# Kernel optimization log

Measured on AMD Instinct MI355X. Metric: run time of the kernel, lower is better.

The kernel has to match this reference:

```python
import jax, jax.numpy as jnp
import numpy as np

N = 100000      # nodes
E = 1600000     # edges (avg degree 16)
DIN = 128
DH = 128
DOUT = 64
K = 2           # SGConv propagation steps
EPS = 1e-5      # BatchNorm eps


def setup_inputs() -> dict:
    key = jax.random.key(0)
    ks = jax.random.split(key, 12)
    x = jax.random.normal(ks[0], (N, DIN), dtype=jnp.float32)
    edge_index = jax.random.randint(ks[1], (2, E), 0, N, dtype=jnp.int32)
    def lin(k, fin, fout):
        k1, k2 = jax.random.split(k)
        s = 1.0 / np.sqrt(fin)
        W = jax.random.uniform(k1, (fin, fout), jnp.float32, -s, s)
        b = jax.random.uniform(k2, (fout,), jnp.float32, -s, s)
        return W, b
    W1, b1 = lin(ks[2], DIN, DH)
    W2, b2 = lin(ks[3], DH, DH)
    W3, b3 = lin(ks[4], DH, DOUT)
    g1 = jnp.ones((DH,), jnp.float32); be1 = jnp.zeros((DH,), jnp.float32)
    g2 = jnp.ones((DH,), jnp.float32); be2 = jnp.zeros((DH,), jnp.float32)
    return {"x": x, "edge_index": edge_index,
            "W1": W1, "b1": b1, "g1": g1, "be1": be1,
            "W2": W2, "b2": b2, "g2": g2, "be2": be2,
            "W3": W3, "b3": b3}


def _sgc_propagate(h, row, col, norm):
    # h: [N, d]; gather source nodes, scale per-edge, scatter-add to dest
    for _ in range(K):
        msg = norm[:, None] * h[row]                      # [E, d]
        h = jax.ops.segment_sum(msg, col, num_segments=N)  # [N, d]
    return h


def _batchnorm(h, gamma, beta):
    # training-mode BN over node axis, biased variance (torch semantics)
    mu = jnp.mean(h, axis=0)
    var = jnp.mean(jnp.square(h - mu), axis=0)
    return gamma * (h - mu) * jax.lax.rsqrt(var + EPS) + beta


def reference(x, edge_index, W1, b1, g1, be1, W2, b2, g2, be2, W3, b3):
    row, col = edge_index[0], edge_index[1]
    # symmetric degree normalization; degree counted on row (as in source)
    deg = jax.ops.segment_sum(jnp.ones((E,), x.dtype), row, num_segments=N)
    dis = jnp.where(deg > 0, 1.0 / jnp.sqrt(jnp.maximum(deg, 1.0)), 0.0)
    norm = dis[row] * dis[col]                             # [E]

    h = _sgc_propagate(x, row, col, norm)
    h = _batchnorm(h @ W1 + b1, g1, be1)   # dropout p=0.0 -> identity
    h = _sgc_propagate(h, row, col, norm)
    h = _batchnorm(h @ W2 + b2, g2, be2)
    return h @ W3 + b3                      # [N, DOUT]
```

## Files before the change

### kernel.cpp

```cpp
#include <hip/hip_runtime.h>


typedef __attribute__((ext_vector_type(8))) short bf16x8;
typedef __attribute__((ext_vector_type(4))) float f32x4;

#define RBITS 12
#define RSIZE (1 << RBITS)
#define NRANGE 25
#define NCHUNK 100
#define RSTRIDE (NRANGE * RSIZE)
#define SLOTS 64

static inline size_t align256(size_t x) { return (x + 255) & ~(size_t)255; }

__device__ inline unsigned short bf16rn(float f) {
    unsigned int u = __builtin_bit_cast(unsigned int, f);
    u += 0x7fffu + ((u >> 16) & 1u);
    return (unsigned short)(u >> 16);
}
__device__ inline float bflo(unsigned int u) { return __builtin_bit_cast(float, u << 16); }
__device__ inline float bfhi(unsigned int u) { return __builtin_bit_cast(float, u & 0xffff0000u); }
__device__ inline unsigned int packbf2(float a, float b) {
    return (unsigned int)bf16rn(a) | ((unsigned int)bf16rn(b) << 16);
}

__global__ void hist_row_kernel(const int* __restrict__ row, int E,
                                int* __restrict__ staging) {
    __shared__ int lcnt[RSIZE];
    int range = blockIdx.x % NRANGE;
    int chunk = blockIdx.x / NRANGE;
    for (int i = threadIdx.x; i < RSIZE; i += 256) lcnt[i] = 0;
    __syncthreads();
    int lo = range << RBITS;
    int ebeg = (int)((long long)E * chunk / NCHUNK);
    int eend = (int)((long long)E * (chunk + 1) / NCHUNK);
    for (int i = ebeg + threadIdx.x * 4; i + 3 < eend; i += 256 * 4) {
        int4 v = *(const int4*)(row + i);
        unsigned a;
        a = (unsigned)(v.x - lo); if (a < RSIZE) atomicAdd(&lcnt[a], 1);
        a = (unsigned)(v.y - lo); if (a < RSIZE) atomicAdd(&lcnt[a], 1);
        a = (unsigned)(v.z - lo); if (a < RSIZE) atomicAdd(&lcnt[a], 1);
        a = (unsigned)(v.w - lo); if (a < RSIZE) atomicAdd(&lcnt[a], 1);
    }
    __syncthreads();
    int* dst = staging + chunk * RSTRIDE + lo;
    for (int i = threadIdx.x; i < RSIZE; i += 256) dst[i] = lcnt[i];
}

__global__ void dis_kernel(const int* __restrict__ staging, float* __restrict__ dis, int n) {
    int i = blockIdx.x * blockDim.x + threadIdx.x;
    if (i < n) {
        int d = 0;
#pragma unroll 4
        for (int c = 0; c < NCHUNK; ++c) d += staging[c * RSTRIDE + i];
        dis[i] = d > 0 ? rsqrtf((float)d) : 0.f;
    }
}

__global__ void bucket_fill_kernel(const int* __restrict__ row, const int* __restrict__ col,
                                   const float* __restrict__ dis,
                                   int* __restrict__ fcnt, int2* __restrict__ bucket, int E) {
    int e = blockIdx.x * blockDim.x + threadIdx.x;
    if (e < E) {
        int r = row[e], c = col[e];
        int slot = atomicAdd(&fcnt[c], 1);
        if (slot < SLOTS) {
            int2 v;
            v.x = r;
            v.y = __float_as_int(dis[r] * dis[c]);
            bucket[(size_t)c * SLOTS + slot] = v;
        }
    }
}


__global__ void xcvt_kernel(const float* __restrict__ x, unsigned int* __restrict__ x16, int total4) {
    for (int i = blockIdx.x * blockDim.x + threadIdx.x; i < total4; i += gridDim.x * blockDim.x) {
        float4 f = ((const float4*)x)[i];
        x16[i * 2] = packbf2(f.x, f.y);
        x16[i * 2 + 1] = packbf2(f.z, f.w);
    }
}

__global__ void wcvt_kernel(const float* __restrict__ W1, const float* __restrict__ W2,
                            unsigned short* __restrict__ W1t, unsigned short* __restrict__ W2t) {
    int i = blockIdx.x * blockDim.x + threadIdx.x;
    if (i < 32768) {
        const float* W = (i < 16384) ? W1 : W2;
        unsigned short* T = (i < 16384) ? W1t : W2t;
        int j = i & 16383;
        int k = j >> 7, c = j & 127;
        T[c * 128 + k] = bf16rn(W[j]);
    }
}


template <bool AFF>
__global__ void spmm16_kernel(const int* __restrict__ fcnt, const int2* __restrict__ bucket,
                              const unsigned short* __restrict__ h_in,
                              const float* __restrict__ scale, const float* __restrict__ shift,
                              unsigned short* __restrict__ h_out, int n) {
    int gw = __builtin_amdgcn_readfirstlane((blockIdx.x * blockDim.x + threadIdx.x) >> 6);
    int lane = threadIdx.x & 63;
    int sub = lane & 15;
    int grp = lane >> 4;
    if (gw >= n) return;
    uint4* outp = (uint4*)(h_out + (size_t)gw * 128) + sub;
    int cnt = fcnt[gw];
    cnt = cnt < SLOTS ? cnt : SLOTS;
    if (cnt == 0) {
        if (lane < 16) {
            uint4 z = {0u, 0u, 0u, 0u};
            *outp = z;
        }
        return;
    }
    const int2* base = bucket + (size_t)gw * SLOTS;
    float acc[8];
#pragma unroll
    for (int j = 0; j < 8; ++j) acc[j] = 0.f;
    float sc[8], sh[8];
    if (AFF) {
        float4 s0 = ((const float4*)scale)[sub * 2];
        float4 s1 = ((const float4*)scale)[sub * 2 + 1];
        float4 h0 = ((const float4*)shift)[sub * 2];
        float4 h1 = ((const float4*)shift)[sub * 2 + 1];
        sc[0] = s0.x; sc[1] = s0.y; sc[2] = s0.z; sc[3] = s0.w;
        sc[4] = s1.x; sc[5] = s1.y; sc[6] = s1.z; sc[7] = s1.w;
        sh[0] = h0.x; sh[1] = h0.y; sh[2] = h0.z; sh[3] = h0.w;
        sh[4] = h1.x; sh[5] = h1.y; sh[6] = h1.z; sh[7] = h1.w;
    }
    bool g1 = (grp & 1) != 0;
    bool g2 = (grp & 2) != 0;
    for (int j0 = 0; j0 < cnt; j0 += 16) {
        int2 ent[16];
#pragma unroll
        for (int k = 0; k < 16; ++k) ent[k] = base[j0 + k];
        uint4 u[4];
        float wsel[4];
#pragma unroll
        for (int k = 0; k < 4; ++k) {
            int i0 = j0 + 4 * k;
            int e0 = (i0 + 0 < cnt) ? ent[4 * k + 0].x : 0;
            int e1 = (i0 + 1 < cnt) ? ent[4 * k + 1].x : 0;
            int e2 = (i0 + 2 < cnt) ? ent[4 * k + 2].x : 0;
            int e3 = (i0 + 3 < cnt) ? ent[4 * k + 3].x : 0;
            float w0 = (i0 + 0 < cnt) ? __int_as_float(ent[4 * k + 0].y) : 0.f;
            float w1 = (i0 + 1 < cnt) ? __int_as_float(ent[4 * k + 1].y) : 0.f;
            float w2 = (i0 + 2 < cnt) ? __int_as_float(ent[4 * k + 2].y) : 0.f;
            float w3 = (i0 + 3 < cnt) ? __int_as_float(ent[4 * k + 3].y) : 0.f;
            int eA = g1 ? e1 : e0;
            int eB = g1 ? e3 : e2;
            int esel = g2 ? eB : eA;
            float wA = g1 ? w1 : w0;
            float wB = g1 ? w3 : w2;
            wsel[k] = g2 ? wB : wA;
            u[k] = *(const uint4*)(h_in + (size_t)esel * 128 + sub * 8);
        }
#pragma unroll
        for (int k = 0; k < 4; ++k) {
            float w = wsel[k];
            unsigned int uu[4] = {u[k].x, u[k].y, u[k].z, u[k].w};
#pragma unroll
            for (int q = 0; q < 4; ++q) {
                float f0 = bflo(uu[q]), f1 = bfhi(uu[q]);
                if (AFF) {
                    f0 = fmaf(sc[2 * q], f0, sh[2 * q]);
                    f1 = fmaf(sc[2 * q + 1], f1, sh[2 * q + 1]);
                }
                acc[2 * q] = fmaf(w, f0, acc[2 * q]);
                acc[2 * q + 1] = fmaf(w, f1, acc[2 * q + 1]);
            }
        }
    }
#pragma unroll
    for (int j = 0; j < 8; ++j) {
        acc[j] += __shfl_xor(acc[j], 16, 64);
        acc[j] += __shfl_xor(acc[j], 32, 64);
    }
    if (lane < 16) {
        uint4 o;
        o.x = packbf2(acc[0], acc[1]);
        o.y = packbf2(acc[2], acc[3]);
        o.z = packbf2(acc[4], acc[5]);
        o.w = packbf2(acc[6], acc[7]);
        *outp = o;
    }
}


template <int NCT, bool OUTF32, bool STATS>
__launch_bounds__(256)
__global__ void gemm16_kernel(const unsigned short* __restrict__ X,
                              const unsigned short* __restrict__ Wt,
                              const float* __restrict__ bias, void* __restrict__ Y,
                              float* __restrict__ gsum, float* __restrict__ gsq, int n) {
    __shared__ __align__(16) char lds[NCT * 16 * 256];
    __shared__ float ssum[NCT * 16], ssq[NCT * 16];
    for (int i = threadIdx.x; i < NCT * 16 * 16; i += 256) {
        int col = i >> 4;
        int kbyte = (i & 15) << 4;
        *(uint4*)(lds + col * 256 + (kbyte ^ ((col & 7) << 4))) = ((const uint4*)Wt)[i];
    }
    if (STATS) {
        for (int i = threadIdx.x; i < NCT * 16; i += 256) {
            ssum[i] = 0.f;
            ssq[i] = 0.f;
        }
    }
    __syncthreads();

    int lane = threadIdx.x & 63;
    int wave = threadIdx.x >> 6;
    int cl = lane & 15, g = lane >> 4;

    bf16x8 b[NCT][4];
#pragma unroll
    for (int ct = 0; ct < NCT; ++ct) {
        int col = ct * 16 + cl;
#pragma unroll
        for (int kc = 0; kc < 4; ++kc) {
            int kbyte = kc * 64 + g * 16;
            b[ct][kc] = *(const bf16x8*)(lds + col * 256 + (kbyte ^ ((col & 7) << 4)));
        }
    }
    float bc[NCT];
#pragma unroll
    for (int ct = 0; ct < NCT; ++ct) bc[ct] = bias[ct * 16 + cl];

    for (int rb0 = blockIdx.x * 64; rb0 < n; rb0 += gridDim.x * 64) {
        int rb = rb0 + wave * 16;
        if (rb >= n) continue;
        int row = rb + cl;
        int rowc = row < n ? row : n - 1;
        const unsigned short* xr = X + (size_t)rowc * 128;
        bf16x8 a[4];
#pragma unroll
        for (int kc = 0; kc < 4; ++kc) a[kc] = *(const bf16x8*)(xr + kc * 32 + g * 8);
#pragma unroll
        for (int ct = 0; ct < NCT; ++ct) {
            f32x4 acc = {bc[ct], bc[ct], bc[ct], bc[ct]};
#pragma unroll
            for (int kc = 0; kc < 4; ++kc)
                acc = __builtin_amdgcn_mfma_f32_16x16x32_bf16(a[kc], b[ct][kc], acc, 0, 0, 0);
            int colo = ct * 16 + cl;
            if (STATS) {
                float s = acc[0] + acc[1] + acc[2] + acc[3];
                float q = acc[0] * acc[0] + acc[1] * acc[1] + acc[2] * acc[2] + acc[3] * acc[3];
                s += __shfl_xor(s, 16, 64);
                s += __shfl_xor(s, 32, 64);
                q += __shfl_xor(q, 16, 64);
                q += __shfl_xor(q, 32, 64);
                if (g == 0) {
                    atomicAdd(&ssum[colo], s);
                    atomicAdd(&ssq[colo], q);
                }
            }
#pragma unroll
            for (int i = 0; i < 4; ++i) {
                int ro = rb + g * 4 + i;
                if (ro < n) {
                    if (OUTF32)
                        ((float*)Y)[(size_t)ro * (NCT * 16) + colo] = acc[i];
                    else
                        ((unsigned short*)Y)[(size_t)ro * 128 + colo] = bf16rn(acc[i]);
                }
            }
        }
    }
    if (STATS) {
        __syncthreads();
        for (int i = threadIdx.x; i < NCT * 16; i += 256) {
            atomicAdd(&gsum[i], ssum[i]);
            atomicAdd(&gsq[i], ssq[i]);
        }
    }
}


__global__ void bn_final_kernel(const float* __restrict__ gsum, const float* __restrict__ gsq,
                                const float* __restrict__ gamma, const float* __restrict__ beta,
                                int n, float* __restrict__ scale, float* __restrict__ shift) {
    int c = threadIdx.x;
    if (c < 128) {
        float fn = (float)n;
        float mu = gsum[c] / fn;
        float var = gsq[c] / fn - mu * mu;
        float inv = rsqrtf(var + 1e-5f);
        float sc = gamma[c] * inv;
        scale[c] = sc;
        shift[c] = beta[c] - sc * mu;
    }
}

__global__ void fold_w3_kernel(const float* __restrict__ W3, const float* __restrict__ b3,
                               const float* __restrict__ scale, const float* __restrict__ shift,
                               unsigned short* __restrict__ W3t, float* __restrict__ b3f) {
    int c = threadIdx.x;
    if (c < 64) {
        float acc = b3[c];
        for (int k = 0; k < 128; ++k) {
            float w = W3[k * 64 + c];
            W3t[c * 128 + k] = bf16rn(scale[k] * w);
            acc += shift[k] * w;
        }
        b3f[c] = acc;
    }
}


extern "C" void kernel_launch(void* const* d_in, const int* in_sizes, int n_in,
                              void* d_out, int out_size, void* d_ws, size_t ws_size,
                              hipStream_t stream) {
    const float* x = (const float*)d_in[0];
    const int* edge = (const int*)d_in[1];
    const float* W1 = (const float*)d_in[2];
    const float* b1 = (const float*)d_in[3];
    const float* g1 = (const float*)d_in[4];
    const float* be1 = (const float*)d_in[5];
    const float* W2 = (const float*)d_in[6];
    const float* b2 = (const float*)d_in[7];
    const float* g2 = (const float*)d_in[8];
    const float* be2 = (const float*)d_in[9];
    const float* W3 = (const float*)d_in[10];
    const float* b3 = (const float*)d_in[11];
    float* out = (float*)d_out;

    const int N = in_sizes[0] / 128;
    const int E = in_sizes[1] / 2;
    const int* erow = edge;
    const int* ecol = edge + E;

    char* p = (char*)d_ws;
    size_t off = 0;
    auto carve = [&](size_t bytes) {
        void* r = p + off;
        off += align256(bytes);
        return r;
    };
    unsigned short* x16 = (unsigned short*)carve((size_t)N * 128 * 2);
    unsigned short* A16 = (unsigned short*)carve((size_t)N * 128 * 2);
    unsigned short* B16 = (unsigned short*)carve((size_t)N * 128 * 2);
    int2* bucket = (int2*)carve((size_t)N * SLOTS * 8);
    int* fcnt = (int*)carve((size_t)N * 4);
    float* dis = (float*)carve((size_t)N * 4);
    float* gsum = (float*)carve(1024);
    float* gsq = (float*)(gsum + 128);
    float* scale1 = (float*)carve(512);
    float* shift1 = (float*)carve(512);
    float* scale2 = (float*)carve(512);
    float* shift2 = (float*)carve(512);
    unsigned short* W1t = (unsigned short*)carve(128 * 128 * 2);
    unsigned short* W2t = (unsigned short*)carve(128 * 128 * 2);
    unsigned short* W3t = (unsigned short*)carve(64 * 128 * 2);
    float* b3f = (float*)carve(256);
    int* staging = (int*)bucket;
    (void)ws_size;

    const int TB = 256;
    const int gE = (E + TB - 1) / TB;
    const int gN = (N + TB - 1) / TB;
    const int gSp = (N + 3) / 4;
    const int gGemm = (N + 63) / 64;
    const int gGemmS = 320;

    hipMemsetAsync(fcnt, 0, (size_t)N * 4, stream);
    hist_row_kernel<<<NRANGE * NCHUNK, TB, 0, stream>>>(erow, E, staging);
    dis_kernel<<<gN, TB, 0, stream>>>(staging, dis, N);
    bucket_fill_kernel<<<gE, TB, 0, stream>>>(erow, ecol, dis, fcnt, bucket, E);

    xcvt_kernel<<<2048, TB, 0, stream>>>(x, (unsigned int*)x16, N * 32);
    wcvt_kernel<<<128, TB, 0, stream>>>(W1, W2, W1t, W2t);

    spmm16_kernel<false><<<gSp, TB, 0, stream>>>(fcnt, bucket, x16, nullptr, nullptr, A16, N);
    spmm16_kernel<false><<<gSp, TB, 0, stream>>>(fcnt, bucket, A16, nullptr, nullptr, B16, N);

    hipMemsetAsync(gsum, 0, 1024, stream);
    gemm16_kernel<8, false, true><<<gGemmS, TB, 0, stream>>>(B16, W1t, b1, A16, gsum, gsq, N);
    bn_final_kernel<<<1, 128, 0, stream>>>(gsum, gsq, g1, be1, N, scale1, shift1);

    spmm16_kernel<true><<<gSp, TB, 0, stream>>>(fcnt, bucket, A16, scale1, shift1, B16, N);
    spmm16_kernel<false><<<gSp, TB, 0, stream>>>(fcnt, bucket, B16, nullptr, nullptr, A16, N);

    hipMemsetAsync(gsum, 0, 1024, stream);
    gemm16_kernel<8, false, true><<<gGemmS, TB, 0, stream>>>(A16, W2t, b2, B16, gsum, gsq, N);
    bn_final_kernel<<<1, 128, 0, stream>>>(gsum, gsq, g2, be2, N, scale2, shift2);

    fold_w3_kernel<<<1, 64, 0, stream>>>(W3, b3, scale2, shift2, W3t, b3f);
    gemm16_kernel<4, true, false><<<gGemm, TB, 0, stream>>>(B16, W3t, b3f, out, nullptr, nullptr, N);
}
```

Measured before the change: 463.7 us.

## Build compact CSR via two-pass partition sort instead of fixed-slot buckets

Replaces the atomic fixed-slot (64 per node) bucket fill with a two-level counting sort: a per-chunk histogram over coarse column buckets, a scan, a scatter into partitions, then a per-bucket local sort that writes a dense CSR with per-edge norms. The SpMM kernels then read contiguous CSR ranges instead of padded slot arrays, which removes global atomics on per-node counters, the memset, and the sparse padded reads. It also drops the 64-edge cap, so high-degree nodes are no longer silently truncated. The row-degree histogram now packs two 16-bit counts per shared word, so each block covers a larger node range and fewer blocks are launched. In exchange it adds several extra kernel launches, including a single-block scan that runs serially.

```diff
diff --git a/kernel.cpp b/kernel.cpp
--- a/kernel.cpp
+++ b/kernel.cpp
@@ -4,12 +4,14 @@
 typedef __attribute__((ext_vector_type(8))) short bf16x8;
 typedef __attribute__((ext_vector_type(4))) float f32x4;
 
-#define RBITS 12
-#define RSIZE (1 << RBITS)
-#define NRANGE 25
-#define NCHUNK 100
-#define RSTRIDE (NRANGE * RSIZE)
-#define SLOTS 64
+#define HR_RBITS 14
+#define HR_RSIZE 16384
+#define HR_NRANGE 7
+#define HR_NCHUNK 100
+#define HR_WPC (HR_NRANGE * HR_RSIZE / 2)
+
+#define PA_NCHUNK 256
+#define PB_SHIFT 8
 
 static inline size_t align256(size_t x) { return (x + 255) & ~(size_t)255; }
 
@@ -25,51 +27,131 @@
 }
 
 __global__ void hist_row_kernel(const int* __restrict__ row, int E,
-                                int* __restrict__ staging) {
-    __shared__ int lcnt[RSIZE];
-    int range = blockIdx.x % NRANGE;
-    int chunk = blockIdx.x / NRANGE;
-    for (int i = threadIdx.x; i < RSIZE; i += 256) lcnt[i] = 0;
-    __syncthreads();
-    int lo = range << RBITS;
-    int ebeg = (int)((long long)E * chunk / NCHUNK);
-    int eend = (int)((long long)E * (chunk + 1) / NCHUNK);
+                                unsigned int* __restrict__ staging) {
+    __shared__ unsigned int l32[HR_RSIZE / 2];
+    int range = blockIdx.x % HR_NRANGE;
+    int chunk = blockIdx.x / HR_NRANGE;
+    for (int i = threadIdx.x; i < HR_RSIZE / 2; i += 256) l32[i] = 0;
+    __syncthreads();
+    int lo = range << HR_RBITS;
+    int ebeg = (int)((long long)E * chunk / HR_NCHUNK);
+    int eend = (int)((long long)E * (chunk + 1) / HR_NCHUNK);
     for (int i = ebeg + threadIdx.x * 4; i + 3 < eend; i += 256 * 4) {
         int4 v = *(const int4*)(row + i);
         unsigned a;
-        a = (unsigned)(v.x - lo); if (a < RSIZE) atomicAdd(&lcnt[a], 1);
-        a = (unsigned)(v.y - lo); if (a < RSIZE) atomicAdd(&lcnt[a], 1);
-        a = (unsigned)(v.z - lo); if (a < RSIZE) atomicAdd(&lcnt[a], 1);
-        a = (unsigned)(v.w - lo); if (a < RSIZE) atomicAdd(&lcnt[a], 1);
-    }
-    __syncthreads();
-    int* dst = staging + chunk * RSTRIDE + lo;
-    for (int i = threadIdx.x; i < RSIZE; i += 256) dst[i] = lcnt[i];
-}
-
-__global__ void dis_kernel(const int* __restrict__ staging, float* __restrict__ dis, int n) {
+        a = (unsigned)(v.x - lo); if (a < HR_RSIZE) atomicAdd(&l32[a >> 1], (a & 1) ? 0x10000u : 1u);
+        a = (unsigned)(v.y - lo); if (a < HR_RSIZE) atomicAdd(&l32[a >> 1], (a & 1) ? 0x10000u : 1u);
+        a = (unsigned)(v.z - lo); if (a < HR_RSIZE) atomicAdd(&l32[a >> 1], (a & 1) ? 0x10000u : 1u);
+        a = (unsigned)(v.w - lo); if (a < HR_RSIZE) atomicAdd(&l32[a >> 1], (a & 1) ? 0x10000u : 1u);
+    }
+    __syncthreads();
+    unsigned int* dst = staging + (size_t)chunk * HR_WPC + (lo >> 1);
+    for (int i = threadIdx.x; i < HR_RSIZE / 2; i += 256) dst[i] = l32[i];
+}
+
+__global__ void dis_kernel(const unsigned int* __restrict__ staging, float* __restrict__ dis, int n) {
     int i = blockIdx.x * blockDim.x + threadIdx.x;
     if (i < n) {
+        int shift = (i & 1) * 16;
         int d = 0;
 #pragma unroll 4
-        for (int c = 0; c < NCHUNK; ++c) d += staging[c * RSTRIDE + i];
+        for (int c = 0; c < HR_NCHUNK; ++c)
+            d += (staging[(size_t)c * HR_WPC + (i >> 1)] >> shift) & 0xffff;
         dis[i] = d > 0 ? rsqrtf((float)d) : 0.f;
     }
 }
 
-__global__ void bucket_fill_kernel(const int* __restrict__ row, const int* __restrict__ col,
-                                   const float* __restrict__ dis,
-                                   int* __restrict__ fcnt, int2* __restrict__ bucket, int E) {
-    int e = blockIdx.x * blockDim.x + threadIdx.x;
-    if (e < E) {
-        int r = row[e], c = col[e];
-        int slot = atomicAdd(&fcnt[c], 1);
-        if (slot < SLOTS) {
-            int2 v;
-            v.x = r;
-            v.y = __float_as_int(dis[r] * dis[c]);
-            bucket[(size_t)c * SLOTS + slot] = v;
-        }
+
+__global__ void pa_hist_kernel(const int* __restrict__ col, int E,
+                               int* __restrict__ chunkhist, int nbuck) {
+    __shared__ int lh[512];
+    int chunk = blockIdx.x;
+    for (int i = threadIdx.x; i < nbuck; i += 256) lh[i] = 0;
+    __syncthreads();
+    int ebeg = (int)((long long)E * chunk / PA_NCHUNK);
+    int eend = (int)((long long)E * (chunk + 1) / PA_NCHUNK);
+    for (int i = ebeg + threadIdx.x; i < eend; i += 256)
+        atomicAdd(&lh[col[i] >> PB_SHIFT], 1);
+    __syncthreads();
+    for (int i = threadIdx.x; i < nbuck; i += 256)
+        chunkhist[i * PA_NCHUNK + chunk] = lh[i];
+}
+
+__global__ void pa_scan_kernel(int* __restrict__ chunkhist, int* __restrict__ bucketstart,
+                               int nbuck) {
+    __shared__ int tot[512];
+    int b = threadIdx.x;
+    if (b < nbuck) {
+        int run = 0;
+        int* p = chunkhist + b * PA_NCHUNK;
+        for (int c = 0; c < PA_NCHUNK; ++c) { int v = p[c]; p[c] = run; run += v; }
+        tot[b] = run;
+    }
+    __syncthreads();
+    if (threadIdx.x == 0) {
+        int run = 0;
+        for (int i = 0; i < nbuck; ++i) { bucketstart[i] = run; run += tot[i]; }
+        bucketstart[nbuck] = run;
+    }
+    __syncthreads();
+    if (b < nbuck) {
+        int base = bucketstart[b];
+        int* p = chunkhist + b * PA_NCHUNK;
+        for (int c = 0; c < PA_NCHUNK; ++c) p[c] += base;
+    }
+}
+
+__global__ void pa_scatter_kernel(const int* __restrict__ row, const int* __restrict__ col,
+                                  int E, const int* __restrict__ chunkhist,
+                                  int2* __restrict__ part, int nbuck) {
+    __shared__ int loff[512];
+    int chunk = blockIdx.x;
+    for (int i = threadIdx.x; i < nbuck; i += 256)
+        loff[i] = chunkhist[i * PA_NCHUNK + chunk];
+    __syncthreads();
+    int ebeg = (int)((long long)E * chunk / PA_NCHUNK);
+    int eend = (int)((long long)E * (chunk + 1) / PA_NCHUNK);
+    for (int i = ebeg + threadIdx.x; i < eend; i += 256) {
+        int r = row[i], c = col[i];
+        int pos = atomicAdd(&loff[c >> PB_SHIFT], 1);
+        int2 v; v.x = r; v.y = c;
+        part[pos] = v;
+    }
+}
+
+__global__ void pb_kernel(const int2* __restrict__ part, const int* __restrict__ bucketstart,
+                          const float* __restrict__ dis, int2* __restrict__ csr,
+                          int* __restrict__ csr_ptr, int n) {
+    __shared__ int lcnt[256], sh[256], loff[256];
+    int b = blockIdx.x, t = threadIdx.x;
+    int nlo = b << PB_SHIFT;
+    int ebeg = bucketstart[b], eend = bucketstart[b + 1];
+    lcnt[t] = 0;
+    __syncthreads();
+    for (int i = ebeg + t; i < eend; i += 256)
+        atomicAdd(&lcnt[part[i].y - nlo], 1);
+    __syncthreads();
+    int v = lcnt[t];
+    sh[t] = v;
+    __syncthreads();
+    for (int off = 1; off < 256; off <<= 1) {
+        int tv = (t >= off) ? sh[t - off] : 0;
+        __syncthreads();
+        sh[t] += tv;
+        __syncthreads();
+    }
+    int excl = sh[t] - v;
+    loff[t] = excl;
+    if (nlo + t <= n) csr_ptr[nlo + t] = ebeg + excl;
+    __syncthreads();
+    for (int i = ebeg + t; i < eend; i += 256) {
+        int2 e = part[i];
+        int c = e.y;
+        int slot = atomicAdd(&loff[c - nlo], 1);
+        int2 o;
+        o.x = e.x;
+        o.y = __float_as_int(dis[e.x] * dis[c]);
+        csr[ebeg + slot] = o;
     }
 }
 
@@ -96,7 +178,7 @@
 
 
 template <bool AFF>
-__global__ void spmm16_kernel(const int* __restrict__ fcnt, const int2* __restrict__ bucket,
+__global__ void spmm16_kernel(const int* __restrict__ csr_ptr, const int2* __restrict__ csr,
                               const unsigned short* __restrict__ h_in,
                               const float* __restrict__ scale, const float* __restrict__ shift,
                               unsigned short* __restrict__ h_out, int n) {
@@ -106,8 +188,9 @@
     int grp = lane >> 4;
     if (gw >= n) return;
     uint4* outp = (uint4*)(h_out + (size_t)gw * 128) + sub;
-    int cnt = fcnt[gw];
-    cnt = cnt < SLOTS ? cnt : SLOTS;
+    int beg = csr_ptr[gw];
+    int end = csr_ptr[gw + 1];
+    int cnt = end - beg;
     if (cnt == 0) {
         if (lane < 16) {
             uint4 z = {0u, 0u, 0u, 0u};
@@ -115,7 +198,7 @@
         }
         return;
     }
-    const int2* base = bucket + (size_t)gw * SLOTS;
+    const int2* base = csr + beg;
     float acc[8];
 #pragma unroll
     for (int j = 0; j < 8; ++j) acc[j] = 0.f;
@@ -330,6 +413,7 @@
     const int E = in_sizes[1] / 2;
     const int* erow = edge;
     const int* ecol = edge + E;
+    const int nbuck = (N + 255) >> PB_SHIFT;
 
     char* p = (char*)d_ws;
     size_t off = 0;
@@ -341,8 +425,11 @@
     unsigned short* x16 = (unsigned short*)carve((size_t)N * 128 * 2);
     unsigned short* A16 = (unsigned short*)carve((size_t)N * 128 * 2);
     unsigned short* B16 = (unsigned short*)carve((size_t)N * 128 * 2);
-    int2* bucket = (int2*)carve((size_t)N * SLOTS * 8);
-    int* fcnt = (int*)carve((size_t)N * 4);
+    int2* part = (int2*)carve((size_t)E * 8);
+    int2* csr = (int2*)carve((size_t)E * 8 + 256);
+    int* csr_ptr = (int*)carve((size_t)(N + 1) * 4);
+    int* chunkhist = (int*)carve((size_t)(nbuck + 1) * PA_NCHUNK * 4);
+    int* bucketstart = (int*)carve((size_t)(nbuck + 1) * 4);
     float* dis = (float*)carve((size_t)N * 4);
     float* gsum = (float*)carve(1024);
     float* gsq = (float*)(gsum + 128);
@@ -354,33 +441,34 @@
     unsigned short* W2t = (unsigned short*)carve(128 * 128 * 2);
     unsigned short* W3t = (unsigned short*)carve(64 * 128 * 2);
     float* b3f = (float*)carve(256);
-    int* staging = (int*)bucket;
+    unsigned int* staging = (unsigned int*)part;
     (void)ws_size;
 
     const int TB = 256;
-    const int gE = (E + TB - 1) / TB;
     const int gN = (N + TB - 1) / TB;
     const int gSp = (N + 3) / 4;
     const int gGemm = (N + 63) / 64;
     const int gGemmS = 320;
 
-    hipMemsetAsync(fcnt, 0, (size_t)N * 4, stream);
-    hist_row_kernel<<<NRANGE * NCHUNK, TB, 0, stream>>>(erow, E, staging);
+    hist_row_kernel<<<HR_NRANGE * HR_NCHUNK, TB, 0, stream>>>(erow, E, staging);
     dis_kernel<<<gN, TB, 0, stream>>>(staging, dis, N);
-    bucket_fill_kernel<<<gE, TB, 0, stream>>>(erow, ecol, dis, fcnt, bucket, E);
+    pa_hist_kernel<<<PA_NCHUNK, TB, 0, stream>>>(ecol, E, chunkhist, nbuck);
+    pa_scan_kernel<<<1, 512, 0, stream>>>(chunkhist, bucketstart, nbuck);
+    pa_scatter_kernel<<<PA_NCHUNK, TB, 0, stream>>>(erow, ecol, E, chunkhist, part, nbuck);
+    pb_kernel<<<nbuck, TB, 0, stream>>>(part, bucketstart, dis, csr, csr_ptr, N);
 
     xcvt_kernel<<<2048, TB, 0, stream>>>(x, (unsigned int*)x16, N * 32);
     wcvt_kernel<<<128, TB, 0, stream>>>(W1, W2, W1t, W2t);
 
-    spmm16_kernel<false><<<gSp, TB, 0, stream>>>(fcnt, bucket, x16, nullptr, nullptr, A16, N);
-    spmm16_kernel<false><<<gSp, TB, 0, stream>>>(fcnt, bucket, A16, nullptr, nullptr, B16, N);
+    spmm16_kernel<false><<<gSp, TB, 0, stream>>>(csr_ptr, csr, x16, nullptr, nullptr, A16, N);
+    spmm16_kernel<false><<<gSp, TB, 0, stream>>>(csr_ptr, csr, A16, nullptr, nullptr, B16, N);
 
     hipMemsetAsync(gsum, 0, 1024, stream);
     gemm16_kernel<8, false, true><<<gGemmS, TB, 0, stream>>>(B16, W1t, b1, A16, gsum, gsq, N);
     bn_final_kernel<<<1, 128, 0, stream>>>(gsum, gsq, g1, be1, N, scale1, shift1);
 
-    spmm16_kernel<true><<<gSp, TB, 0, stream>>>(fcnt, bucket, A16, scale1, shift1, B16, N);
-    spmm16_kernel<false><<<gSp, TB, 0, stream>>>(fcnt, bucket, B16, nullptr, nullptr, A16, N);
+    spmm16_kernel<true><<<gSp, TB, 0, stream>>>(csr_ptr, csr, A16, scale1, shift1, B16, N);
+    spmm16_kernel<false><<<gSp, TB, 0, stream>>>(csr_ptr, csr, B16, nullptr, nullptr, A16, N);
 
     hipMemsetAsync(gsum, 0, 1024, stream);
     gemm16_kernel<8, false, true><<<gGemmS, TB, 0, stream>>>(A16, W2t, b2, B16, gsum, gsq, N);
```

Result: no change. 458.2 us (-1.2%).
